# Optimization experiments

Hardware: AMD Instinct MI355X
Metric: run time of the kernel (lower is better)

The kernel has to match this reference:

```python
import jax, jax.numpy as jnp
import numpy as np

B, S, T, E, H = 2, 2048, 2048, 1024, 16
HD = E // H  # head_dim = 64


def setup_inputs() -> dict:
    key = jax.random.key(0)
    ks = jax.random.split(key, 12)
    sc = 1.0 / np.sqrt(E)
    inp = {
        "query": jax.random.normal(ks[0], (B, S, E), jnp.float32),
        "key": jax.random.normal(ks[1], (B, T, E), jnp.float32),
        "value": jax.random.normal(ks[2], (B, T, E), jnp.float32),
        "attn_mask": jnp.ones((S, T), jnp.int32),
        # nn.Linear params: y = x @ W.T + b
        "Wq": jax.random.normal(ks[3], (E, E), jnp.float32) * sc,
        "bq": jax.random.normal(ks[4], (E,), jnp.float32) * sc,
        "Wk": jax.random.normal(ks[5], (E, E), jnp.float32) * sc,
        "bk": jax.random.normal(ks[6], (E,), jnp.float32) * sc,
        "Wv": jax.random.normal(ks[7], (E, E), jnp.float32) * sc,
        "bv": jax.random.normal(ks[8], (E,), jnp.float32) * sc,
        "Wo": jax.random.normal(ks[9], (E, E), jnp.float32) * sc,
        "bo": jax.random.normal(ks[10], (E,), jnp.float32) * sc,
    }
    return inp


def reference(query, key, value, attn_mask, Wq, bq, Wk, bk, Wv, bv, Wo, bo):
    N, Sq, Ed = query.shape
    Tk = key.shape[1]
    # projections (torch Linear: x @ W.T + b)
    q = query @ Wq.T + bq
    k = key @ Wk.T + bk
    v = value @ Wv.T + bv
    # split heads -> (N, H, S, HD)
    q = q.reshape(N, Sq, H, HD).transpose(0, 2, 1, 3)
    k = k.reshape(N, Tk, H, HD).transpose(0, 2, 1, 3)
    v = v.reshape(N, Tk, H, HD).transpose(0, 2, 1, 3)
    # scaled dot-product scores: (N, H, S, T)
    energy = jnp.einsum("nhsd,nhtd->nhst", q, k) / jnp.sqrt(jnp.float32(HD))
    energy = jnp.where(attn_mask[None, None, :, :] == 0, -jnp.inf, energy)
    attn = jax.nn.softmax(energy, axis=3)
    # dropout is identity in eval mode
    out = jnp.einsum("nhst,nhtd->nshd", attn, v).reshape(N, Sq, Ed)
    return out @ Wo.T + bo
```

## Files before the change

### kernel.cpp

```cpp
#include <hip/hip_runtime.h>

typedef __attribute__((ext_vector_type(8))) short short8;
typedef __attribute__((ext_vector_type(4))) float f32x4;
typedef __attribute__((ext_vector_type(16))) float f32x16;

#define DEV __device__ __forceinline__

constexpr int Bb = 2, Ss = 2048, Tt = 2048, Ee = 1024, Hh = 16, HDd = 64;
constexpr int Mm = Bb * Ss;
constexpr size_t NX = (size_t)Mm * Ee;
constexpr size_t NW = (size_t)Ee * Ee;

constexpr size_t OFF_WQ   = 0;
constexpr size_t OFF_WK   = OFF_WQ + NW * 2;
constexpr size_t OFF_WV   = OFF_WK + NW * 2;
constexpr size_t OFF_WO   = OFF_WV + NW * 2;
constexpr size_t OFF_QH   = OFF_WO + NW * 2;
constexpr size_t OFF_KH   = OFF_QH + NX * 2;
constexpr size_t OFF_VH   = OFF_KH + NX * 2;
constexpr size_t OFF_OB   = OFF_VH + NX * 2;
constexpr size_t OFF_FLAG = OFF_OB + NX * 2;

DEV unsigned short f2bf(float f) {
  union { float f; unsigned u; } v; v.f = f;
  unsigned r = v.u + 0x7fffu + ((v.u >> 16) & 1u);
  return (unsigned short)(r >> 16);
}

#define GLDS16(g, l) __builtin_amdgcn_global_load_lds(                         \
    (const __attribute__((address_space(1))) void*)(g),                        \
    (__attribute__((address_space(3))) void*)(l), 16, 0, 0)

#define PLSWAP(a, b) asm("v_permlane32_swap_b32 %0, %1" : "+v"(a), "+v"(b))
#define CVTPK(d, lo, hi_) asm("v_cvt_pk_bf16_f32 %0, %1, %2" : "=v"(d) : "v"(lo), "v"(hi_))

#if __has_builtin(__builtin_amdgcn_exp2f)
#define EXP2(x) __builtin_amdgcn_exp2f(x)
#else
#define EXP2(x) __expf((x) * 0.69314718f)
#endif

constexpr float SCLQ = 0.18033688f;

__global__ __launch_bounds__(256) void prep_kernel(
    const float* __restrict__ wq, const float* __restrict__ wk,
    const float* __restrict__ wv, const float* __restrict__ wo,
    const int* __restrict__ mask,
    unsigned short* __restrict__ Wqb, unsigned short* __restrict__ Wkb,
    unsigned short* __restrict__ Wvb, unsigned short* __restrict__ Wob,
    int* __restrict__ flagZero)
{
  constexpr size_t NWv = NW / 4, NXv = NX / 4;
  constexpr size_t tot = 4 * NWv + NXv;
  for (size_t u = (size_t)blockIdx.x * blockDim.x + threadIdx.x; u < tot;
       u += (size_t)gridDim.x * blockDim.x) {
    if (u < 4 * NWv) {
      int wsel = (int)(u / NWv); size_t off = u % NWv;
      const float* src = wsel == 0 ? wq : wsel == 1 ? wk : wsel == 2 ? wv : wo;
      unsigned short* dst = wsel == 0 ? Wqb : wsel == 1 ? Wkb : wsel == 2 ? Wvb : Wob;
      float4 f = ((const float4*)src)[off];
      ushort4 o; o.x = f2bf(f.x); o.y = f2bf(f.y); o.z = f2bf(f.z); o.w = f2bf(f.w);
      ((ushort4*)dst)[off] = o;
    } else {
      size_t off = u - 4 * NWv;
      int4 m = ((const int4*)mask)[off];
      if (m.x == 0 || m.y == 0 || m.z == 0 || m.w == 0) *flagZero = 1;
    }
  }
}

DEV void gemm128_f32A(const float* __restrict__ Af, const unsigned short* __restrict__ Bm,
                      unsigned short (*Asm)[128 * 32], unsigned short (*Bsm)[128 * 32],
                      f32x4 acc[4][4], int K)
{
  const int t = threadIdx.x;
  const int w = t >> 6, lane = t & 63;
  const int l15 = lane & 15, l4 = lane >> 4;
  const int wm = w >> 1, wn = w & 1;
  const int srow = lane >> 2;
  const int skc  = (lane & 3) * 8;
  const int ar = t >> 2;
  const int ak = (t & 3) * 8;
#pragma unroll
  for (int mi = 0; mi < 4; ++mi)
#pragma unroll
    for (int ni = 0; ni < 4; ++ni) acc[mi][ni] = (f32x4){0.f, 0.f, 0.f, 0.f};

  float4 x0, x1, x2, x3;
  float4 y0, y1, y2, y3;

#define ALOAD(r0, r1, r2, r3, k0)                                            \
  { const float* ap  = Af + (size_t)ar * K + (k0) + ak;                      \
    const float* ap2 = ap + (size_t)64 * K;                                  \
    r0 = *(const float4*)ap;  r1 = *(const float4*)(ap + 4);                 \
    r2 = *(const float4*)ap2; r3 = *(const float4*)(ap2 + 4); }
#define BSTAGE(d, k0)                                                        \
  { GLDS16(Bm + (size_t)(w * 16 + srow) * K + (k0) + skc,      Bsm[d] + w * 512);        \
    GLDS16(Bm + (size_t)(64 + w * 16 + srow) * K + (k0) + skc, Bsm[d] + 2048 + w * 512); }
#define AWRITE(d, r0, r1, r2, r3)                                            \
  { unsigned u0, u1, u2, u3, u4, u5, u6, u7;                                 \
    CVTPK(u0, r0.x, r0.y); CVTPK(u1, r0.z, r0.w);                            \
    CVTPK(u2, r1.x, r1.y); CVTPK(u3, r1.z, r1.w);                            \
    CVTPK(u4, r2.x, r2.y); CVTPK(u5, r2.z, r2.w);                            \
    CVTPK(u6, r3.x, r3.y); CVTPK(u7, r3.z, r3.w);                            \
    union { unsigned u[4]; short8 s; } p0, p1;                               \
    p0.u[0] = u0; p0.u[1] = u1; p0.u[2] = u2; p0.u[3] = u3;                  \
    p1.u[0] = u4; p1.u[1] = u5; p1.u[2] = u6; p1.u[3] = u7;                  \
    *(short8*)&Asm[d][ar * 32 + ak]        = p0.s;                           \
    *(short8*)&Asm[d][(64 + ar) * 32 + ak] = p1.s; }
#define COMP(cur)                                                            \
  { short8 af[4], bf[4];                                                     \
    _Pragma("unroll")                                                        \
    for (int mi = 0; mi < 4; ++mi)                                           \
      af[mi] = *(const short8*)&Asm[cur][(wm * 64 + mi * 16 + l15) * 32 + l4 * 8]; \
    _Pragma("unroll")                                                        \
    for (int ni = 0; ni < 4; ++ni)                                           \
      bf[ni] = *(const short8*)&Bsm[cur][(wn * 64 + ni * 16 + l15) * 32 + l4 * 8]; \
    __builtin_amdgcn_s_setprio(1);                                           \
    _Pragma("unroll")                                                        \
    for (int mi = 0; mi < 4; ++mi)                                           \
      _Pragma("unroll")                                                      \
      for (int ni = 0; ni < 4; ++ni)                                         \
        acc[mi][ni] = __builtin_amdgcn_mfma_f32_16x16x32_bf16(af[mi], bf[ni], acc[mi][ni], 0, 0, 0); \
    __builtin_amdgcn_s_setprio(0); }

  ALOAD(x0, x1, x2, x3, 0)
  BSTAGE(0, 0)
  asm volatile("s_waitcnt vmcnt(2)" ::: "memory");
  AWRITE(0, x0, x1, x2, x3)
  ALOAD(y0, y1, y2, y3, 32)
  asm volatile("s_waitcnt vmcnt(4)" ::: "memory");
  asm volatile("s_waitcnt lgkmcnt(0)" ::: "memory");
  __builtin_amdgcn_s_barrier();

  const int nt = K / 32;
  for (int tt = 0; tt + 2 < nt; tt += 2) {
    BSTAGE(1, (tt + 1) * 32)
    ALOAD(x0, x1, x2, x3, (tt + 2) * 32)
    COMP(0)
    asm volatile("s_waitcnt vmcnt(4)" ::: "memory");
    AWRITE(1, y0, y1, y2, y3)
    asm volatile("s_waitcnt lgkmcnt(0)" ::: "memory");
    __builtin_amdgcn_s_barrier();
    BSTAGE(0, (tt + 2) * 32)
    ALOAD(y0, y1, y2, y3, (tt + 3) * 32)
    COMP(1)
    asm volatile("s_waitcnt vmcnt(4)" ::: "memory");
    AWRITE(0, x0, x1, x2, x3)
    asm volatile("s_waitcnt lgkmcnt(0)" ::: "memory");
    __builtin_amdgcn_s_barrier();
  }
  BSTAGE(1, (nt - 1) * 32)
  COMP(0)
  asm volatile("s_waitcnt vmcnt(2)" ::: "memory");
  AWRITE(1, y0, y1, y2, y3)
  asm volatile("s_waitcnt lgkmcnt(0)" ::: "memory");
  __builtin_amdgcn_s_barrier();
  asm volatile("s_waitcnt vmcnt(0)" ::: "memory");
  COMP(1)
#undef ALOAD
#undef BSTAGE
#undef AWRITE
#undef COMP
}

DEV void gemm128_8w(const unsigned short* __restrict__ A, const unsigned short* __restrict__ Bm,
                    unsigned short (*Asm)[128 * 32], unsigned short (*Bsm)[128 * 32],
                    f32x4 acc[2][4], int K)
{
  const int tid = threadIdx.x, w = tid >> 6, lane = tid & 63;
  const int l15 = lane & 15, l4 = lane >> 4;
  const int wm = w >> 1, wn = w & 1;
  const int grow = tid >> 2, gk = (tid & 3) * 8;
#pragma unroll
  for (int mi = 0; mi < 2; ++mi)
#pragma unroll
    for (int ni = 0; ni < 4; ++ni) acc[mi][ni] = (f32x4){0.f, 0.f, 0.f, 0.f};

#define GSTAGE8(d, k0)                                                   \
  {                                                                      \
    GLDS16(A  + (size_t)grow * K + (k0) + gk, Asm[d] + w * 512);         \
    GLDS16(Bm + (size_t)grow * K + (k0) + gk, Bsm[d] + w * 512);         \
  }

  GSTAGE8(0, 0)
  int it = 0;
  for (int k0 = 0; k0 < K; k0 += 32, ++it) {
    const int cur = it & 1;
    asm volatile("s_waitcnt vmcnt(0)" ::: "memory");
    __builtin_amdgcn_s_barrier();
    if (k0 + 32 < K) GSTAGE8(cur ^ 1, k0 + 32)

    short8 af[2], bf[4];
#pragma unroll
    for (int mi = 0; mi < 2; ++mi)
      af[mi] = *(const short8*)&Asm[cur][(wm * 32 + mi * 16 + l15) * 32 + l4 * 8];
#pragma unroll
    for (int ni = 0; ni < 4; ++ni)
      bf[ni] = *(const short8*)&Bsm[cur][(wn * 64 + ni * 16 + l15) * 32 + l4 * 8];
    __builtin_amdgcn_s_setprio(1);
#pragma unroll
    for (int mi = 0; mi < 2; ++mi)
#pragma unroll
      for (int ni = 0; ni < 4; ++ni)
        acc[mi][ni] = __builtin_amdgcn_mfma_f32_16x16x32_bf16(af[mi], bf[ni], acc[mi][ni], 0, 0, 0);
    __builtin_amdgcn_s_setprio(0);
  }
#undef GSTAGE8
}

__global__ __launch_bounds__(256, 3) void gemm_qkv(
    const float* __restrict__ q, const float* __restrict__ k, const float* __restrict__ v,
    const unsigned short* __restrict__ Wqb, const unsigned short* __restrict__ Wkb,
    const unsigned short* __restrict__ Wvb,
    const float* __restrict__ bq, const float* __restrict__ bk, const float* __restrict__ bv,
    unsigned short* __restrict__ Qh, unsigned short* __restrict__ Kh, unsigned short* __restrict__ Vh)
{
  __shared__ unsigned short Asm[2][128 * 32], Bsm[2][128 * 32];
  const int orig = (blockIdx.z * 32 + blockIdx.y) * 8 + blockIdx.x;
  const int sid  = (orig & 7) * 96 + (orig >> 3);
  const int z  = sid >> 8;
  const int by = (sid & 255) >> 3, bx = sid & 7;
  const float* A           = (z == 0) ? q   : (z == 1) ? k   : v;
  const unsigned short* Bw = (z == 0) ? Wqb : (z == 1) ? Wkb : Wvb;
  const float* bias        = (z == 0) ? bq  : (z == 1) ? bk  : bv;
  unsigned short* Out      = (z == 0) ? Qh  : (z == 1) ? Kh  : Vh;
  f32x4 acc[4][4];
  gemm128_f32A(A + (size_t)by * 128 * Ee, Bw + (size_t)bx * 128 * Ee, Asm, Bsm, acc, Ee);
  const int t = threadIdx.x, w = t >> 6, lane = t & 63, l15 = lane & 15, l4 = lane >> 4;
  const int wm = w >> 1, wn = w & 1;
  if (z < 2) {
    const float osc = (z == 0) ? SCLQ : 1.0f;
#pragma unroll
    for (int ni = 0; ni < 4; ++ni) {
      int col = bx * 128 + wn * 64 + ni * 16 + l15;
      float bcol = bias[col];
      int h = col >> 6, hd = col & 63;
#pragma unroll
      for (int mi = 0; mi < 4; ++mi) {
#pragma unroll
        for (int r = 0; r < 4; ++r) {
          int row = by * 128 + wm * 64 + mi * 16 + l4 * 4 + r;
          int b = row >> 11, s = row & 2047;
          Out[(((size_t)(b * Hh + h)) * Ss + s) * HDd + hd] = f2bf((acc[mi][ni][r] + bcol) * osc);
        }
      }
    }
  } else {
#pragma unroll
    for (int ni = 0; ni < 4; ++ni) {
      int col = bx * 128 + wn * 64 + ni * 16 + l15;
      float bcol = bias[col];
      int h = col >> 6, hd = col & 63;
#pragma unroll
      for (int mi = 0; mi < 4; ++mi) {
        int row = by * 128 + wm * 64 + mi * 16 + l4 * 4;
        int b = row >> 11, s = row & 2047;
        ushort4 pk;
        pk.x = f2bf(acc[mi][ni][0] + bcol); pk.y = f2bf(acc[mi][ni][1] + bcol);
        pk.z = f2bf(acc[mi][ni][2] + bcol); pk.w = f2bf(acc[mi][ni][3] + bcol);
        *(ushort4*)&Out[((size_t)((b * Hh + h) * HDd + hd)) * Ss + s] = pk;
      }
    }
  }
}

__global__ __launch_bounds__(512) void gemm_out(
    const unsigned short* __restrict__ Ob, const unsigned short* __restrict__ Wob,
    const float* __restrict__ bo, float* __restrict__ out)
{
  __shared__ unsigned short Asm[2][128 * 32], Bsm[2][128 * 32];
  const int orig = blockIdx.y * 8 + blockIdx.x;
  const int sid  = (orig & 7) * 32 + (orig >> 3);
  const int by = sid >> 3, bx = sid & 7;
  f32x4 acc[2][4];
  gemm128_8w(Ob + (size_t)by * 128 * Ee, Wob + (size_t)bx * 128 * Ee, Asm, Bsm, acc, Ee);
  const int tid = threadIdx.x, w = tid >> 6, lane = tid & 63;
  const int l15 = lane & 15, l4 = lane >> 4;
  const int wm = w >> 1, wn = w & 1;
#pragma unroll
  for (int ni = 0; ni < 4; ++ni) {
    int col = bx * 128 + wn * 64 + ni * 16 + l15;
    float bcol = bo[col];
#pragma unroll
    for (int mi = 0; mi < 2; ++mi) {
#pragma unroll
      for (int r = 0; r < 4; ++r) {
        int row = by * 128 + wm * 32 + mi * 16 + l4 * 4 + r;
        out[(size_t)row * Ee + col] = acc[mi][ni][r] + bcol;
      }
    }
  }
}

__global__ __launch_bounds__(256, 4) void attn_kernel(
    const unsigned short* __restrict__ Qh, const unsigned short* __restrict__ Kh,
    const unsigned short* __restrict__ Vh, const int* __restrict__ mask,
    const int* __restrict__ flagZero, unsigned short* __restrict__ Ob)
{
  __shared__ unsigned short Ks[2][64 * 64];
  __shared__ unsigned short Vs[2][64 * 64];
  const int bh = blockIdx.y, qt = blockIdx.x;
  const int tid = threadIdx.x, w = tid >> 6, lane = tid & 63;
  const int l31 = lane & 31, hi = lane >> 5;
  const int g = w >> 1, p = w & 1;
  const bool useMask = (*flagZero != 0);
  const size_t bhBase = (size_t)bh * Ss * HDd;
  const int s0 = qt * 64 + g * 32;
  const int trow = p * 32 + l31;

  short8 qf[4];
#pragma unroll
  for (int ks = 0; ks < 4; ++ks)
    qf[ks] = *(const short8*)&Qh[bhBase + (size_t)(s0 + l31) * 64 + ks * 16 + hi * 8];

  f32x16 o0, o1, Z16;
#pragma unroll
  for (int r = 0; r < 16; ++r) { o0[r] = 0.f; o1[r] = 0.f; Z16[r] = 0.f; }
  float l_r = 0.f;

  const int cRow = tid >> 3, cG = (tid & 7) ^ (cRow & 7);

#define STAGE(d, kt2)                                                                         \
  {                                                                                           \
    _Pragma("unroll")                                                                         \
    for (int i = 0; i < 2; ++i)                                                               \
      GLDS16(Kh + bhBase + (size_t)((kt2) + i * 32 + cRow) * 64 + cG * 8,                     \
             &Ks[d][0] + (i * 256 + w * 64) * 8);                                             \
    _Pragma("unroll")                                                                         \
    for (int i = 0; i < 2; ++i)                                                               \
      GLDS16(Vh + bhBase + (size_t)(i * 32 + cRow) * Ss + (kt2) + cG * 8,                     \
             &Vs[d][0] + (i * 256 + w * 64) * 8);                                             \
  }

#define SMPACK(kt2)                                                                           \
  {                                                                                           \
    if (useMask) {                                                                            \
      int sg = s0 + l31;                                                                      \
      _Pragma("unroll")                                                                       \
      for (int r = 0; r < 16; ++r) {                                                          \
        int tg = (kt2) + p * 32 + (r & 3) + 8 * (r >> 2) + 4 * hi;                            \
        if (mask[(size_t)sg * Tt + tg] == 0) pr[r] = -1e30f;                                  \
      }                                                                                       \
    }                                                                                         \
    _Pragma("unroll")                                                                         \
    for (int r = 0; r < 16; ++r) pr[r] = EXP2(pr[r]);                                         \
    float a0 = (pr[0] + pr[1]) + (pr[2] + pr[3]);                                             \
    float a1 = (pr[4] + pr[5]) + (pr[6] + pr[7]);                                             \
    float a2 = (pr[8] + pr[9]) + (pr[10] + pr[11]);                                           \
    float a3 = (pr[12] + pr[13]) + (pr[14] + pr[15]);                                         \
    l_r += (a0 + a1) + (a2 + a3);                                                             \
    _Pragma("unroll")                                                                         \
    for (int h2 = 0; h2 < 2; ++h2) {                                                          \
      unsigned c0, c1, d0, d1; const int bse = h2 * 8;                                        \
      CVTPK(c0, pr[bse + 0], pr[bse + 1]);                                                    \
      CVTPK(c1, pr[bse + 2], pr[bse + 3]);                                                    \
      CVTPK(d0, pr[bse + 4], pr[bse + 5]);                                                    \
      CVTPK(d1, pr[bse + 6], pr[bse + 7]);                                                    \
      PLSWAP(c0, d0); PLSWAP(c1, d1);                                                         \
      union { unsigned u[4]; short8 s; } cc;                                                  \
      cc.u[0] = c0; cc.u[1] = c1; cc.u[2] = d0; cc.u[3] = d1;                                 \
      pa[h2] = cc.s;                                                                          \
    }                                                                                         \
  }

  f32x16 pr;
  short8 pa[2];

  STAGE(0, 0)
  asm volatile("s_waitcnt vmcnt(2)" ::: "memory");
  __builtin_amdgcn_s_barrier();
  STAGE(1, 64)
  {
    const unsigned short* Kc = &Ks[0][0];
    short8 ka = *(const short8*)&Kc[trow * 64 + ((hi ^ (l31 & 7)) * 8)];
    pr = __builtin_amdgcn_mfma_f32_32x32x16_bf16(ka, qf[0], Z16, 0, 0, 0);
#pragma unroll
    for (int ks = 1; ks < 4; ++ks) {
      short8 kb = *(const short8*)&Kc[trow * 64 + (((ks * 2 + hi) ^ (l31 & 7)) * 8)];
      pr = __builtin_amdgcn_mfma_f32_32x32x16_bf16(kb, qf[ks], pr, 0, 0, 0);
    }
  }
  SMPACK(0)

  for (int t = 0; t < 32; ++t) {
    const int cur = t & 1;
    if (t < 31) { asm volatile("s_waitcnt vmcnt(2)" ::: "memory"); }
    else        { asm volatile("s_waitcnt vmcnt(0)" ::: "memory"); }
    __builtin_amdgcn_s_barrier();

    const unsigned short* Vc = &Vs[cur][0];
    __builtin_amdgcn_s_setprio(1);
    if (t < 31) {
      const unsigned short* Kn = &Ks[cur ^ 1][0];
      short8 ka0 = *(const short8*)&Kn[trow * 64 + (((0 + hi) ^ (l31 & 7)) * 8)];
      short8 ka1 = *(const short8*)&Kn[trow * 64 + (((2 + hi) ^ (l31 & 7)) * 8)];
      short8 ka2 = *(const short8*)&Kn[trow * 64 + (((4 + hi) ^ (l31 & 7)) * 8)];
      short8 ka3 = *(const short8*)&Kn[trow * 64 + (((6 + hi) ^ (l31 & 7)) * 8)];
      short8 vf00 = *(const short8*)&Vc[l31 * 64 + (((p * 4 + 0 + hi) ^ (l31 & 7)) * 8)];
      short8 vf01 = *(const short8*)&Vc[(32 + l31) * 64 + (((p * 4 + 0 + hi) ^ ((l31 & 7))) * 8)];
      short8 vf10 = *(const short8*)&Vc[l31 * 64 + (((p * 4 + 2 + hi) ^ (l31 & 7)) * 8)];
      short8 vf11 = *(const short8*)&Vc[(32 + l31) * 64 + (((p * 4 + 2 + hi) ^ ((l31 & 7))) * 8)];
      f32x16 prN;
      prN = __builtin_amdgcn_mfma_f32_32x32x16_bf16(ka0, qf[0], Z16, 0, 0, 0);
      o0  = __builtin_amdgcn_mfma_f32_32x32x16_bf16(pa[0], vf00, o0, 0, 0, 0);
      o1  = __builtin_amdgcn_mfma_f32_32x32x16_bf16(pa[0], vf01, o1, 0, 0, 0);
      prN = __builtin_amdgcn_mfma_f32_32x32x16_bf16(ka1, qf[1], prN, 0, 0, 0);
      o0  = __builtin_amdgcn_mfma_f32_32x32x16_bf16(pa[1], vf10, o0, 0, 0, 0);
      prN = __builtin_amdgcn_mfma_f32_32x32x16_bf16(ka2, qf[2], prN, 0, 0, 0);
      o1  = __builtin_amdgcn_mfma_f32_32x32x16_bf16(pa[1], vf11, o1, 0, 0, 0);
      prN = __builtin_amdgcn_mfma_f32_32x32x16_bf16(ka3, qf[3], prN, 0, 0, 0);
      pr = prN;
    } else {
      short8 vf00 = *(const short8*)&Vc[l31 * 64 + (((p * 4 + 0 + hi) ^ (l31 & 7)) * 8)];
      short8 vf01 = *(const short8*)&Vc[(32 + l31) * 64 + (((p * 4 + 0 + hi) ^ ((l31 & 7))) * 8)];
      short8 vf10 = *(const short8*)&Vc[l31 * 64 + (((p * 4 + 2 + hi) ^ (l31 & 7)) * 8)];
      short8 vf11 = *(const short8*)&Vc[(32 + l31) * 64 + (((p * 4 + 2 + hi) ^ ((l31 & 7))) * 8)];
      o0 = __builtin_amdgcn_mfma_f32_32x32x16_bf16(pa[0], vf00, o0, 0, 0, 0);
      o1 = __builtin_amdgcn_mfma_f32_32x32x16_bf16(pa[0], vf01, o1, 0, 0, 0);
      o0 = __builtin_amdgcn_mfma_f32_32x32x16_bf16(pa[1], vf10, o0, 0, 0, 0);
      o1 = __builtin_amdgcn_mfma_f32_32x32x16_bf16(pa[1], vf11, o1, 0, 0, 0);
    }
    __builtin_amdgcn_s_setprio(0);

    if (t < 31) SMPACK((t + 1) * 64)

    __builtin_amdgcn_s_barrier();
    if (t < 30) STAGE(cur, (t + 2) * 64)
  }
#undef STAGE
#undef SMPACK

  __syncthreads();

  float* Ox = (float*)&Ks[0][0];
  float* Ml = (float*)&Vs[0][0];
  float lt = l_r + __shfl_xor(l_r, 32);
  if (p == 1) {
#pragma unroll
    for (int r = 0; r < 16; ++r) {
      int sr = (r & 3) + 8 * (r >> 2) + 4 * hi;
      Ox[g * 2048 + sr * 64 + l31]      = o0[r];
      Ox[g * 2048 + sr * 64 + 32 + l31] = o1[r];
    }
    if (hi == 0) Ml[g * 32 + l31] = lt;
  }
  __syncthreads();
  if (p == 0) {
    const int b = bh >> 4, h = bh & 15;
    float ltot = lt + Ml[g * 32 + l31];
    float linv = ltot > 0.f ? 1.0f / ltot : 0.f;
#pragma unroll
    for (int r = 0; r < 16; ++r) {
      int sr = (r & 3) + 8 * (r >> 2) + 4 * hi;
      float li = __shfl(linv, sr);
      size_t rowbase = (size_t)(b * Ss + s0 + sr) * Ee + h * 64;
      Ob[rowbase + l31]      = f2bf((o0[r] + Ox[g * 2048 + sr * 64 + l31]) * li);
      Ob[rowbase + 32 + l31] = f2bf((o1[r] + Ox[g * 2048 + sr * 64 + 32 + l31]) * li);
    }
  }
}

extern "C" void kernel_launch(void* const* d_in, const int* in_sizes, int n_in,
                              void* d_out, int out_size, void* d_ws, size_t ws_size,
                              hipStream_t stream) {
  const float* q   = (const float*)d_in[0];
  const float* k   = (const float*)d_in[1];
  const float* v   = (const float*)d_in[2];
  const int*  msk  = (const int*)d_in[3];
  const float* Wq  = (const float*)d_in[4];
  const float* bq  = (const float*)d_in[5];
  const float* Wk  = (const float*)d_in[6];
  const float* bk  = (const float*)d_in[7];
  const float* Wv  = (const float*)d_in[8];
  const float* bv  = (const float*)d_in[9];
  const float* Wo  = (const float*)d_in[10];
  const float* bo  = (const float*)d_in[11];
  float* out = (float*)d_out;

  char* ws = (char*)d_ws;
  unsigned short* Wqb = (unsigned short*)(ws + OFF_WQ);
  unsigned short* Wkb = (unsigned short*)(ws + OFF_WK);
  unsigned short* Wvb = (unsigned short*)(ws + OFF_WV);
  unsigned short* Wob = (unsigned short*)(ws + OFF_WO);
  unsigned short* Qh  = (unsigned short*)(ws + OFF_QH);
  unsigned short* Kh  = (unsigned short*)(ws + OFF_KH);
  unsigned short* Vh  = (unsigned short*)(ws + OFF_VH);
  unsigned short* Ob  = (unsigned short*)(ws + OFF_OB);
  int* flagZero       = (int*)(ws + OFF_FLAG);

  hipMemsetAsync(flagZero, 0, 4, stream);
  prep_kernel<<<2048, 256, 0, stream>>>(Wq, Wk, Wv, Wo, msk,
                                        Wqb, Wkb, Wvb, Wob, flagZero);
  gemm_qkv<<<dim3(8, 32, 3), 256, 0, stream>>>(q, k, v, Wqb, Wkb, Wvb,
                                               bq, bk, bv, Qh, Kh, Vh);
  attn_kernel<<<dim3(32, 32), 256, 0, stream>>>(Qh, Kh, Vh, msk, flagZero, Ob);
  gemm_out<<<dim3(8, 32), 512, 0, stream>>>(Ob, Wob, bo, out);
}
```

Measured before the change: 124.7 us.

## Use 8-wave blocks for QKV GEMM and remap attention blocks across XCDs

```diff
diff --git a/kernel.cpp b/kernel.cpp
--- a/kernel.cpp
+++ b/kernel.cpp
@@ -69,95 +69,71 @@
   }
 }
 
-DEV void gemm128_f32A(const float* __restrict__ Af, const unsigned short* __restrict__ Bm,
-                      unsigned short (*Asm)[128 * 32], unsigned short (*Bsm)[128 * 32],
-                      f32x4 acc[4][4], int K)
-{
-  const int t = threadIdx.x;
-  const int w = t >> 6, lane = t & 63;
+DEV void gemm128_f32A_8w(const float* __restrict__ Af, const unsigned short* __restrict__ Bm,
+                         unsigned short (*Asm)[128 * 32], unsigned short (*Bsm)[128 * 32],
+                         f32x4 acc[2][4], int K)
+{
+  const int tid = threadIdx.x, w = tid >> 6, lane = tid & 63;
   const int l15 = lane & 15, l4 = lane >> 4;
   const int wm = w >> 1, wn = w & 1;
-  const int srow = lane >> 2;
-  const int skc  = (lane & 3) * 8;
-  const int ar = t >> 2;
-  const int ak = (t & 3) * 8;
-#pragma unroll
-  for (int mi = 0; mi < 4; ++mi)
+  const int ar = tid >> 2;
+  const int ak = (tid & 3) * 8;
+#pragma unroll
+  for (int mi = 0; mi < 2; ++mi)
 #pragma unroll
     for (int ni = 0; ni < 4; ++ni) acc[mi][ni] = (f32x4){0.f, 0.f, 0.f, 0.f};
 
-  float4 x0, x1, x2, x3;
-  float4 y0, y1, y2, y3;
-
-#define ALOAD(r0, r1, r2, r3, k0)                                            \
-  { const float* ap  = Af + (size_t)ar * K + (k0) + ak;                      \
-    const float* ap2 = ap + (size_t)64 * K;                                  \
-    r0 = *(const float4*)ap;  r1 = *(const float4*)(ap + 4);                 \
-    r2 = *(const float4*)ap2; r3 = *(const float4*)(ap2 + 4); }
+  float4 a0, a1;
+#define ALOAD(k0)                                                            \
+  { const float* ap = Af + (size_t)ar * K + (k0) + ak;                       \
+    a0 = *(const float4*)ap; a1 = *(const float4*)(ap + 4); }
 #define BSTAGE(d, k0)                                                        \
-  { GLDS16(Bm + (size_t)(w * 16 + srow) * K + (k0) + skc,      Bsm[d] + w * 512);        \
-    GLDS16(Bm + (size_t)(64 + w * 16 + srow) * K + (k0) + skc, Bsm[d] + 2048 + w * 512); }
-#define AWRITE(d, r0, r1, r2, r3)                                            \
-  { unsigned u0, u1, u2, u3, u4, u5, u6, u7;                                 \
-    CVTPK(u0, r0.x, r0.y); CVTPK(u1, r0.z, r0.w);                            \
-    CVTPK(u2, r1.x, r1.y); CVTPK(u3, r1.z, r1.w);                            \
-    CVTPK(u4, r2.x, r2.y); CVTPK(u5, r2.z, r2.w);                            \
-    CVTPK(u6, r3.x, r3.y); CVTPK(u7, r3.z, r3.w);                            \
-    union { unsigned u[4]; short8 s; } p0, p1;                               \
+  { GLDS16(Bm + (size_t)ar * K + (k0) + ak, Bsm[d] + w * 512); }
+#define AWRITE(d)                                                            \
+  { unsigned u0, u1, u2, u3;                                                 \
+    CVTPK(u0, a0.x, a0.y); CVTPK(u1, a0.z, a0.w);                            \
+    CVTPK(u2, a1.x, a1.y); CVTPK(u3, a1.z, a1.w);                            \
+    union { unsigned u[4]; short8 s; } p0;                                   \
     p0.u[0] = u0; p0.u[1] = u1; p0.u[2] = u2; p0.u[3] = u3;                  \
-    p1.u[0] = u4; p1.u[1] = u5; p1.u[2] = u6; p1.u[3] = u7;                  \
-    *(short8*)&Asm[d][ar * 32 + ak]        = p0.s;                           \
-    *(short8*)&Asm[d][(64 + ar) * 32 + ak] = p1.s; }
+    *(short8*)&Asm[d][ar * 32 + ak] = p0.s; }
 #define COMP(cur)                                                            \
-  { short8 af[4], bf[4];                                                     \
+  { short8 af[2], bf[4];                                                     \
     _Pragma("unroll")                                                        \
-    for (int mi = 0; mi < 4; ++mi)                                           \
-      af[mi] = *(const short8*)&Asm[cur][(wm * 64 + mi * 16 + l15) * 32 + l4 * 8]; \
+    for (int mi = 0; mi < 2; ++mi)                                           \
+      af[mi] = *(const short8*)&Asm[cur][(wm * 32 + mi * 16 + l15) * 32 + l4 * 8]; \
     _Pragma("unroll")                                                        \
     for (int ni = 0; ni < 4; ++ni)                                           \
       bf[ni] = *(const short8*)&Bsm[cur][(wn * 64 + ni * 16 + l15) * 32 + l4 * 8]; \
     __builtin_amdgcn_s_setprio(1);                                           \
     _Pragma("unroll")                                                        \
-    for (int mi = 0; mi < 4; ++mi)                                           \
+    for (int mi = 0; mi < 2; ++mi)                                           \
       _Pragma("unroll")                                                      \
       for (int ni = 0; ni < 4; ++ni)                                         \
         acc[mi][ni] = __builtin_amdgcn_mfma_f32_16x16x32_bf16(af[mi], bf[ni], acc[mi][ni], 0, 0, 0); \
     __builtin_amdgcn_s_setprio(0); }
 
-  ALOAD(x0, x1, x2, x3, 0)
+  ALOAD(0)
   BSTAGE(0, 0)
-  asm volatile("s_waitcnt vmcnt(2)" ::: "memory");
-  AWRITE(0, x0, x1, x2, x3)
-  ALOAD(y0, y1, y2, y3, 32)
-  asm volatile("s_waitcnt vmcnt(4)" ::: "memory");
+  asm volatile("s_waitcnt vmcnt(1)" ::: "memory");
+  AWRITE(0)
   asm volatile("s_waitcnt lgkmcnt(0)" ::: "memory");
+  asm volatile("s_waitcnt vmcnt(0)" ::: "memory");
   __builtin_amdgcn_s_barrier();
 
   const int nt = K / 32;
-  for (int tt = 0; tt + 2 < nt; tt += 2) {
-    BSTAGE(1, (tt + 1) * 32)
-    ALOAD(x0, x1, x2, x3, (tt + 2) * 32)
-    COMP(0)
-    asm volatile("s_waitcnt vmcnt(4)" ::: "memory");
-    AWRITE(1, y0, y1, y2, y3)
-    asm volatile("s_waitcnt lgkmcnt(0)" ::: "memory");
+  for (int t = 0; t < nt; ++t) {
+    const int cur = t & 1;
+    const bool more = (t + 1 < nt);
+    if (more) { ALOAD((t + 1) * 32) BSTAGE(cur ^ 1, (t + 1) * 32) }
+    COMP(cur)
+    if (more) {
+      asm volatile("s_waitcnt vmcnt(1)" ::: "memory");
+      AWRITE(cur ^ 1)
+      asm volatile("s_waitcnt lgkmcnt(0)" ::: "memory");
+      asm volatile("s_waitcnt vmcnt(0)" ::: "memory");
+    }
     __builtin_amdgcn_s_barrier();
-    BSTAGE(0, (tt + 2) * 32)
-    ALOAD(y0, y1, y2, y3, (tt + 3) * 32)
-    COMP(1)
-    asm volatile("s_waitcnt vmcnt(4)" ::: "memory");
-    AWRITE(0, x0, x1, x2, x3)
-    asm volatile("s_waitcnt lgkmcnt(0)" ::: "memory");
-    __builtin_amdgcn_s_barrier();
-  }
-  BSTAGE(1, (nt - 1) * 32)
-  COMP(0)
-  asm volatile("s_waitcnt vmcnt(2)" ::: "memory");
-  AWRITE(1, y0, y1, y2, y3)
-  asm volatile("s_waitcnt lgkmcnt(0)" ::: "memory");
-  __builtin_amdgcn_s_barrier();
-  asm volatile("s_waitcnt vmcnt(0)" ::: "memory");
-  COMP(1)
+  }
 #undef ALOAD
 #undef BSTAGE
 #undef AWRITE
@@ -209,7 +185,7 @@
 #undef GSTAGE8
 }
 
-__global__ __launch_bounds__(256, 3) void gemm_qkv(
+__global__ __launch_bounds__(512) void gemm_qkv(
     const float* __restrict__ q, const float* __restrict__ k, const float* __restrict__ v,
     const unsigned short* __restrict__ Wqb, const unsigned short* __restrict__ Wkb,
     const unsigned short* __restrict__ Wvb,
@@ -225,9 +201,10 @@
   const unsigned short* Bw = (z == 0) ? Wqb : (z == 1) ? Wkb : Wvb;
   const float* bias        = (z == 0) ? bq  : (z == 1) ? bk  : bv;
   unsigned short* Out      = (z == 0) ? Qh  : (z == 1) ? Kh  : Vh;
-  f32x4 acc[4][4];
-  gemm128_f32A(A + (size_t)by * 128 * Ee, Bw + (size_t)bx * 128 * Ee, Asm, Bsm, acc, Ee);
-  const int t = threadIdx.x, w = t >> 6, lane = t & 63, l15 = lane & 15, l4 = lane >> 4;
+  f32x4 acc[2][4];
+  gemm128_f32A_8w(A + (size_t)by * 128 * Ee, Bw + (size_t)bx * 128 * Ee, Asm, Bsm, acc, Ee);
+  const int tid = threadIdx.x, w = tid >> 6, lane = tid & 63;
+  const int l15 = lane & 15, l4 = lane >> 4;
   const int wm = w >> 1, wn = w & 1;
   if (z < 2) {
     const float osc = (z == 0) ? SCLQ : 1.0f;
@@ -237,10 +214,10 @@
       float bcol = bias[col];
       int h = col >> 6, hd = col & 63;
 #pragma unroll
-      for (int mi = 0; mi < 4; ++mi) {
+      for (int mi = 0; mi < 2; ++mi) {
 #pragma unroll
         for (int r = 0; r < 4; ++r) {
-          int row = by * 128 + wm * 64 + mi * 16 + l4 * 4 + r;
+          int row = by * 128 + wm * 32 + mi * 16 + l4 * 4 + r;
           int b = row >> 11, s = row & 2047;
           Out[(((size_t)(b * Hh + h)) * Ss + s) * HDd + hd] = f2bf((acc[mi][ni][r] + bcol) * osc);
         }
@@ -253,8 +230,8 @@
       float bcol = bias[col];
       int h = col >> 6, hd = col & 63;
 #pragma unroll
-      for (int mi = 0; mi < 4; ++mi) {
-        int row = by * 128 + wm * 64 + mi * 16 + l4 * 4;
+      for (int mi = 0; mi < 2; ++mi) {
+        int row = by * 128 + wm * 32 + mi * 16 + l4 * 4;
         int b = row >> 11, s = row & 2047;
         ushort4 pk;
         pk.x = f2bf(acc[mi][ni][0] + bcol); pk.y = f2bf(acc[mi][ni][1] + bcol);
@@ -300,7 +277,10 @@
 {
   __shared__ unsigned short Ks[2][64 * 64];
   __shared__ unsigned short Vs[2][64 * 64];
-  const int bh = blockIdx.y, qt = blockIdx.x;
+  const int orig = blockIdx.y * 32 + blockIdx.x;
+  const int slot = orig >> 3;
+  const int bh = (orig & 7) * 4 + (slot >> 5);
+  const int qt = slot & 31;
   const int tid = threadIdx.x, w = tid >> 6, lane = tid & 63;
   const int l31 = lane & 31, hi = lane >> 5;
   const int g = w >> 1, p = w & 1;
@@ -492,7 +472,7 @@
   hipMemsetAsync(flagZero, 0, 4, stream);
   prep_kernel<<<2048, 256, 0, stream>>>(Wq, Wk, Wv, Wo, msk,
                                         Wqb, Wkb, Wvb, Wob, flagZero);
-  gemm_qkv<<<dim3(8, 32, 3), 256, 0, stream>>>(q, k, v, Wqb, Wkb, Wvb,
+  gemm_qkv<<<dim3(8, 32, 3), 512, 0, stream>>>(q, k, v, Wqb, Wkb, Wvb,
                                                bq, bk, bv, Qh, Kh, Vh);
   attn_kernel<<<dim3(32, 32), 256, 0, stream>>>(Qh, Kh, Vh, msk, flagZero, Ob);
   gemm_out<<<dim3(8, 32), 512, 0, stream>>>(Ob, Wob, bo, out);
```

New measurement: 122.2 us. -2.0%, faster.
